# Kernel optimization log

Measured on AMD Instinct MI355X. Metric: run time of the kernel, lower is better.

The kernel has to match this reference:

```python
import jax, jax.numpy as jnp
import numpy as np

N = 4608      # total nodes (48 graphs x 96 nodes)
B = 48
NPG = 96
D = 512       # vec_dim
XD = 16       # x_dim
E = N * 32    # GAT edges
L = 6         # GAT layers


def _w(k, shape, fan_in):
    return jax.random.normal(k, shape, jnp.float32) * (1.0 / np.sqrt(fan_in))


def setup_inputs() -> dict:
    key = jax.random.key(0)
    ks = jax.random.split(key, 24)
    x = jax.random.normal(ks[0], (N, XD), jnp.float32)
    xyz = jax.random.normal(ks[1], (N, 3), jnp.float32)
    edge_index = jax.random.randint(ks[2], (2, E), 0, N, dtype=jnp.int32)
    ptr = (jnp.arange(B + 1) * NPG).astype(jnp.int32)
    # complete graph with replacement per segment (torch.combinations order: i<=j)
    i, j = np.triu_indices(NPG)
    offs = (np.arange(B) * NPG)[:, None]
    cloud_edge_index = jnp.asarray(
        np.stack([(i[None, :] + offs).reshape(-1), (j[None, :] + offs).reshape(-1)]),
        jnp.int32)
    return {
        'x': x, 'edge_index': edge_index, 'ptr': ptr, 'xyz': xyz,
        'cloud_edge_index': cloud_edge_index,
        'x_proj_w': _w(ks[3], (XD, D), XD), 'x_proj_b': jnp.zeros((D,), jnp.float32),
        'gat_wl': _w(ks[4], (L, D, D), D), 'gat_bl': jnp.zeros((L, D), jnp.float32),
        'gat_wr': _w(ks[5], (L, D, D), D), 'gat_br': jnp.zeros((L, D), jnp.float32),
        'gat_att': _w(ks[6], (L, D), D), 'gat_bias': jnp.zeros((L, D), jnp.float32),
        'gat_ln_g': jnp.ones((L - 1, D), jnp.float32), 'gat_ln_b': jnp.zeros((L - 1, D), jnp.float32),
        'cg_xyz_w': _w(ks[7], (3, D), 3),
        'cg_bn_g': jnp.ones((D,), jnp.float32), 'cg_bn_b': jnp.zeros((D,), jnp.float32),
        'cg_lin1_w': _w(ks[8], (D, D), D), 'cg_lin1_b': jnp.zeros((D,), jnp.float32),
        'cg_ln_g': jnp.ones((D,), jnp.float32), 'cg_ln_b': jnp.zeros((D,), jnp.float32),
        'lin_w': _w(ks[9], (D, D), D), 'lin_b': jnp.zeros((D,), jnp.float32),
        'bn_g': jnp.ones((D,), jnp.float32), 'bn_b': jnp.zeros((D,), jnp.float32),
    }


def _batchnorm(t, g, b):
    mu = t.mean(0)
    v = ((t - mu) ** 2).mean(0)
    return (t - mu) / jnp.sqrt(v + 1e-5) * g + b


def _forward(x, edge_index, cloud_edge_index, x_proj_w, x_proj_b, gat_wl, gat_bl,
             gat_wr, gat_br, gat_att, gat_bias, gat_ln_g, gat_ln_b, cg_xyz_w,
             cg_bn_g, cg_bn_b, cg_lin1_w, cg_lin1_b, cg_ln_g, cg_ln_b,
             lin_w, lin_b, bn_g, bn_b, xyz):
    n = x.shape[0]
    h = x @ x_proj_w + x_proj_b  # [N, D]
    # ---- GATv2 stack (heads=1, self-loops added, eval mode: no dropout) ----
    loops = jnp.arange(n, dtype=edge_index.dtype)
    ei = jnp.concatenate([edge_index, jnp.stack([loops, loops])], axis=1)
    src, dst = ei[0], ei[1]
    xg = h
    for l in range(L):
        xl = xg @ gat_wl[l] + gat_bl[l]
        xr = xg @ gat_wr[l] + gat_br[l]
        e = jax.nn.leaky_relu(xl[src] + xr[dst], 0.2) @ gat_att[l]  # [E+N]
        m = jax.ops.segment_max(e, dst, num_segments=n)
        ew = jnp.exp(e - m[dst])
        den = jax.ops.segment_sum(ew, dst, num_segments=n)
        alpha = ew / den[dst]
        out = jax.ops.segment_sum(alpha[:, None] * xl[src], dst, num_segments=n) + gat_bias[l]
        if l < L - 1:
            # PyG LayerNorm, mode='graph', batch=None: normalize over all elements
            mu = out.mean()
            sd = jnp.sqrt(((out - mu) ** 2).mean())
            out = (out - mu) / (sd + 1e-5) * gat_ln_g[l] + gat_ln_b[l]
            out = jax.nn.relu(out)
        xg = out
    # ---- CloudGraph (complete graph gather-compute-scatter) ----
    a, b = cloud_edge_index[0], cloud_edge_index[1]
    rx = h[a] - h[b]          # [Ec, D]
    rz = xyz[a] - xyz[b]      # [Ec, 3]
    sq = (rz ** 2).sum(-1)
    dist = jnp.where(sq > 0, jnp.sqrt(jnp.where(sq > 0, sq, 1.0)), 0.0)
    w = jnp.exp(-dist)[:, None]
    p1 = jax.ops.segment_sum(jax.nn.relu((w * rx) @ cg_lin1_w + cg_lin1_b), a, num_segments=n)
    mu1 = p1.mean(-1, keepdims=True)
    v1 = ((p1 - mu1) ** 2).mean(-1, keepdims=True)
    ln1 = (p1 - mu1) / jnp.sqrt(v1 + 1e-5) * cg_ln_g + cg_ln_b
    p2 = jax.ops.segment_sum(jax.nn.relu(rz @ cg_xyz_w), a, num_segments=n)
    xc = h + ln1 + _batchnorm(p2, cg_bn_g, cg_bn_b)
    # ---- fuse + final norm ----
    return _batchnorm((h + xg + xc) @ lin_w + lin_b, bn_g, bn_b)


def reference(x, edge_index, ptr, xyz, cloud_edge_index, x_proj_w, x_proj_b,
              gat_wl, gat_bl, gat_wr, gat_br, gat_att, gat_bias, gat_ln_g,
              gat_ln_b, cg_xyz_w, cg_bn_g, cg_bn_b, cg_lin1_w, cg_lin1_b,
              cg_ln_g, cg_ln_b, lin_w, lin_b, bn_g, bn_b):
    return _forward(x, edge_index, cloud_edge_index, x_proj_w, x_proj_b, gat_wl,
                    gat_bl, gat_wr, gat_br, gat_att, gat_bias, gat_ln_g,
                    gat_ln_b, cg_xyz_w, cg_bn_g, cg_bn_b, cg_lin1_w, cg_lin1_b,
                    cg_ln_g, cg_ln_b, lin_w, lin_b, bn_g, bn_b, xyz)
```

## Files before the change

kernel.cpp:

```cpp
#include <hip/hip_runtime.h>
#include <hip/hip_bf16.h>

#define NN 4608
#define BG 48
#define NPG 96
#define DD 512
#define XDIM 16
#define EREAL 147456
#define NLAYER 6
#define NK 262144
#define TRIU 4656

typedef __hip_bfloat16 bf16;
typedef short short8 __attribute__((ext_vector_type(8)));
typedef short shortx4 __attribute__((ext_vector_type(4)));
typedef float f32x4 __attribute__((ext_vector_type(4)));
typedef float f32x2 __attribute__((ext_vector_type(2)));

__device__ __forceinline__ float s2f(short s) {
  return __uint_as_float(((unsigned int)(unsigned short)s) << 16);
}
__device__ __forceinline__ short f2bs(float f) {
  bf16 h = __float2bfloat16(f);
  short s;
  __builtin_memcpy(&s, &h, 2);
  return s;
}
__device__ __forceinline__ void f8x4(unsigned int w, float* o) {
  f32x2 a = __builtin_amdgcn_cvt_pk_f32_fp8(w, false);
  f32x2 b = __builtin_amdgcn_cvt_pk_f32_fp8(w, true);
  o[0] = a[0]; o[1] = a[1]; o[2] = b[0]; o[3] = b[1];
}

typedef const __attribute__((address_space(1))) unsigned int ga_u32;
typedef __attribute__((address_space(3))) unsigned int ls_u32;
__device__ __forceinline__ void gl16(const void* g, void* l) {
  __builtin_amdgcn_global_load_lds((ga_u32*)g, (ls_u32*)l, 16, 0, 0);
}

__global__ __launch_bounds__(256) void k_wt(const float* __restrict__ wl,
                                            const float* __restrict__ wr,
                                            const float* __restrict__ cg,
                                            const float* __restrict__ lin,
                                            bf16* __restrict__ Wt,
                                            int* __restrict__ counts,
                                            float* __restrict__ statsAll) {
  if (blockIdx.z == 0) {
    int id = (blockIdx.y * 16 + blockIdx.x) * 256 + threadIdx.x;
    if (id < NN) counts[id] = 0;
    if (id < 5 * 32) statsAll[id] = 0.f;
  }
  __shared__ float tile[32][33];
  int z = blockIdx.z;
  const float* src = (z < 6) ? wl + (size_t)z * NK
                   : (z < 12) ? wr + (size_t)(z - 6) * NK
                   : (z == 12) ? cg : lin;
  bf16* dst = Wt + (size_t)z * NK;
  int c = threadIdx.x & 31;
  int r0 = threadIdx.x >> 5;
  int bx = blockIdx.x * 32, by = blockIdx.y * 32;
#pragma unroll
  for (int i = 0; i < 4; i++) {
    int r = r0 + i * 8;
    tile[r][c] = src[(size_t)(by + r) * 512 + bx + c];
  }
  __syncthreads();
#pragma unroll
  for (int i = 0; i < 4; i++) {
    int r = r0 + i * 8;
    dst[(size_t)(bx + r) * 512 + by + c] = __float2bfloat16(tile[c][r]);
  }
}

__global__ void k_xproj(const float* __restrict__ x, const float* __restrict__ w,
                        const float* __restrict__ b, const int* __restrict__ ei,
                        const float* __restrict__ xyz,
                        bf16* __restrict__ h_bf, int* __restrict__ counts,
                        float* __restrict__ ep) {
  int i = blockIdx.x * blockDim.x + threadIdx.x;
  if (i >= NN * DD) return;
  if (i < EREAL) atomicAdd(&counts[ei[EREAL + i]], 1);
  if (i < NN * NPG) {
    int n = i / NPG, e = i - n * NPG;
    int p = n % NPG;
    if (e < NPG - p) {
      int g = n / NPG;
      int slot = g * TRIU + p * NPG - (p * (p - 1)) / 2 + e;
      int j = n + e;
      float dx = xyz[n * 3] - xyz[j * 3];
      float dy = xyz[n * 3 + 1] - xyz[j * 3 + 1];
      float dz = xyz[n * 3 + 2] - xyz[j * 3 + 2];
      float sq = dx * dx + dy * dy + dz * dz;
      float dist = (sq > 0.f) ? sqrtf(sq) : 0.f;
      float4 v;
      v.x = dx; v.y = dy; v.z = dz; v.w = __expf(-dist);
      *(float4*)&ep[(size_t)slot * 4] = v;
    }
  }
  int n = i >> 9, d = i & 511;
  float acc = b[d];
#pragma unroll
  for (int k = 0; k < XDIM; k++) acc += x[n * XDIM + k] * w[k * DD + d];
  h_bf[i] = __float2bfloat16(acc);
}

__global__ void k_scan(const int* __restrict__ counts, int* offsets, int* cursor) {
  __shared__ int part[256];
  __shared__ int pre[256];
  int t = threadIdx.x;
  int base = t * 18;
  int s = 0;
#pragma unroll
  for (int i = 0; i < 18; i++) s += counts[base + i];
  part[t] = s;
  __syncthreads();
  if (t == 0) {
    int r = 0;
    for (int i = 0; i < 256; i++) { pre[i] = r; r += part[i]; }
  }
  __syncthreads();
  int run = pre[t];
#pragma unroll
  for (int i = 0; i < 18; i++) {
    offsets[base + i] = run;
    cursor[base + i] = run;
    run += counts[base + i];
  }
  if (t == 0) offsets[NN] = EREAL;
}
__global__ void k_scatter(const int* __restrict__ ei, int* cursor, int* ssrc) {
  int e = blockIdx.x * blockDim.x + threadIdx.x;
  if (e < EREAL) {
    int s = ei[e], d = ei[EREAL + e];
    int pos = atomicAdd(&cursor[d], 1);
    ssrc[pos] = s;
  }
}

__global__ __launch_bounds__(256) void k_ln(const bf16* __restrict__ in,
                                            bf16* __restrict__ out,
                                            const float* __restrict__ stats,
                                            const float* __restrict__ g,
                                            const float* __restrict__ b) {
  float s = 0.f, ss = 0.f;
#pragma unroll
  for (int i = 0; i < 16; i++) { s += stats[i]; ss += stats[16 + i]; }
  const float invM = 1.f / ((float)NN * (float)DD);
  float mu = s * invM;
  float var = ss * invM - mu * mu;
  float sd = sqrtf(fmaxf(var, 0.f));
  float inv = 1.f / (sd + 1e-5f);
  int i = blockIdx.x * 256 + threadIdx.x;
  int base = i * 8;
  int d0 = base & 511;
  short8 raw = *(const short8*)&in[base];
  short8 pk;
#pragma unroll
  for (int k = 0; k < 8; k++) {
    float t = fmaxf((s2f(raw[k]) - mu) * inv * g[d0 + k] + b[d0 + k], 0.f);
    pk[k] = f2bs(t);
  }
  *(short8*)&out[base] = pk;
}

__global__ __launch_bounds__(256) void k_gemm(
    const bf16* __restrict__ Abf,
    const bf16* __restrict__ B0, const bf16* __restrict__ B1,
    const float* __restrict__ bias0, const float* __restrict__ bias1,
    float* __restrict__ C0, float* __restrict__ C1,
    bf16* __restrict__ Cb0, bf16* __restrict__ Cb1,
    unsigned char* __restrict__ Cf8_0, unsigned char* __restrict__ Cf8_1,
    float* __restrict__ zptr, int zn,
    float* __restrict__ csum, float* __restrict__ csq, int nzl) {
  if (zptr && blockIdx.x == 0) {
    for (int i = threadIdx.x; i < zn; i += 256) zptr[i] = 0.f;
  }
  __shared__ __align__(16) bf16 As[2][128 * 64];
  __shared__ __align__(16) bf16 Bs[2][64 * 64];
  __shared__ float cs[64], cq[64];
  int cpx = gridDim.x >> 3;
  int wgid = (blockIdx.x & 7) * cpx + (blockIdx.x >> 3);
  int mi = wgid >> nzl;
  int r = wgid & ((1 << nzl) - 1);
  int z = r >> 3;
  int m0 = mi * 128, n0 = (r & 7) * 64;

  const bf16* B = z ? B1 : B0;
  const float* bias = z ? bias1 : bias0;
  float* C = z ? C1 : C0;
  bf16* Cb = z ? Cb1 : Cb0;
  unsigned char* Cf8 = z ? Cf8_1 : Cf8_0;
  int tid = threadIdx.x;
  int lane = tid & 63, wid = tid >> 6;
  int mh = (wid >> 1) * 64, nh = (wid & 1) * 32;
  int l15 = lane & 15, quad = lane >> 4;
  int lr8 = lane >> 3;
  int ls8 = lane & 7;
  int c16l = ls8 ^ (lr8 & 7);
  int swzr = (l15 & 7) * 8;

  if (csum && tid < 64) { cs[tid] = 0.f; cq[tid] = 0.f; }

  const bf16* aSrc = Abf + (size_t)(m0 + wid * 32 + lr8) * 512 + c16l * 8;
  const bf16* bSrc = B   + (size_t)(n0 + wid * 16 + lr8) * 512 + c16l * 8;

#define STAGE(bi, kt) do {                                              \
    gl16(aSrc + (kt) * 64,            &As[bi][(wid * 32     ) * 64]);   \
    gl16(aSrc + (kt) * 64 +  8 * 512, &As[bi][(wid * 32 +  8) * 64]);   \
    gl16(aSrc + (kt) * 64 + 16 * 512, &As[bi][(wid * 32 + 16) * 64]);   \
    gl16(aSrc + (kt) * 64 + 24 * 512, &As[bi][(wid * 32 + 24) * 64]);   \
    gl16(bSrc + (kt) * 64,            &Bs[bi][(wid * 16     ) * 64]);   \
    gl16(bSrc + (kt) * 64 +  8 * 512, &Bs[bi][(wid * 16 +  8) * 64]);   \
  } while (0)

  f32x4 acc[4][2];
#pragma unroll
  for (int mt = 0; mt < 4; mt++)
#pragma unroll
    for (int nt = 0; nt < 2; nt++) acc[mt][nt] = (f32x4)0.f;

  STAGE(0, 0);
  __syncthreads();

#pragma unroll
  for (int kt = 0; kt < 8; kt++) {
    const int cur = kt & 1;
    if (kt < 7) STAGE(cur ^ 1, kt + 1);
    short8 af[2][4], bfr[2][2];
#pragma unroll
    for (int kk = 0; kk < 2; kk++) {
#pragma unroll
      for (int mt = 0; mt < 4; mt++)
        af[kk][mt] = *(const short8*)&As[cur][(mh + mt * 16 + l15) * 64 +
                                             (((kk * 4 + quad) * 8) ^ swzr)];
#pragma unroll
      for (int nt = 0; nt < 2; nt++)
        bfr[kk][nt] = *(const short8*)&Bs[cur][(nh + nt * 16 + l15) * 64 +
                                              (((kk * 4 + quad) * 8) ^ swzr)];
    }
#pragma unroll
    for (int kk = 0; kk < 2; kk++)
#pragma unroll
      for (int mt = 0; mt < 4; mt++)
#pragma unroll
        for (int nt = 0; nt < 2; nt++)
          acc[mt][nt] = __builtin_amdgcn_mfma_f32_16x16x32_bf16(
              bfr[kk][nt], af[kk][mt], acc[mt][nt], 0, 0, 0);
    __syncthreads();
  }
#undef STAGE

  float colS[2][4] = {{0.f,0.f,0.f,0.f},{0.f,0.f,0.f,0.f}};
  float colQ[2][4] = {{0.f,0.f,0.f,0.f},{0.f,0.f,0.f,0.f}};
  float bv[2][4] = {{0.f,0.f,0.f,0.f},{0.f,0.f,0.f,0.f}};
#pragma unroll
  for (int nt = 0; nt < 2; nt++) {
    if (bias) {
      float4 b4 = *(const float4*)&bias[n0 + nh + nt * 16 + quad * 4];
      bv[nt][0] = b4.x; bv[nt][1] = b4.y; bv[nt][2] = b4.z; bv[nt][3] = b4.w;
    }
  }
#pragma unroll
  for (int mt = 0; mt < 4; mt++) {
    int row = m0 + mh + mt * 16 + l15;
#pragma unroll
    for (int nt = 0; nt < 2; nt++) {
      int col0 = n0 + nh + nt * 16 + quad * 4;
      float v[4];
#pragma unroll
      for (int r2 = 0; r2 < 4; r2++) {
        v[r2] = acc[mt][nt][r2] + bv[nt][r2];
        if (csum) { colS[nt][r2] += v[r2]; colQ[nt][r2] += v[r2] * v[r2]; }
      }
      if (C) {
        float4 o; o.x = v[0]; o.y = v[1]; o.z = v[2]; o.w = v[3];
        *(float4*)&C[(size_t)row * 512 + col0] = o;
      }
      if (Cb) {
        shortx4 o;
#pragma unroll
        for (int r2 = 0; r2 < 4; r2++) o[r2] = f2bs(v[r2]);
        *(shortx4*)&Cb[(size_t)row * 512 + col0] = o;
      }
      if (Cf8) {
        unsigned int u = __builtin_amdgcn_cvt_pk_fp8_f32(v[0], v[1], 0, false);
        u = __builtin_amdgcn_cvt_pk_fp8_f32(v[2], v[3], u, true);
        *(unsigned int*)&Cf8[(size_t)row * 512 + col0] = u;
      }
    }
  }
  if (csum) {
#pragma unroll
    for (int nt = 0; nt < 2; nt++)
#pragma unroll
      for (int r2 = 0; r2 < 4; r2++) {
        atomicAdd(&cs[nh + nt * 16 + quad * 4 + r2], colS[nt][r2]);
        atomicAdd(&cq[nh + nt * 16 + quad * 4 + r2], colQ[nt][r2]);
      }
    __syncthreads();
    if (tid < 64) {
      atomicAdd(&csum[n0 + tid], cs[tid]);
      atomicAdd(&csq[n0 + tid], cq[tid]);
    }
  }
}

__global__ __launch_bounds__(256) void k_gat_edge(const unsigned char* __restrict__ xl8,
                                                  const bf16* __restrict__ xr,
                                                  const float* __restrict__ att,
                                                  const float* __restrict__ bias,
                                                  const int* __restrict__ offs,
                                                  const int* __restrict__ ssrc,
                                                  bf16* __restrict__ out,
                                                  float* __restrict__ statsOut) {
  __shared__ float redS[4], redSS[4];
  int wave = (blockIdx.x * blockDim.x + threadIdx.x) >> 6;
  int lane = threadIdx.x & 63;
  int wid = threadIdx.x >> 6;
  if (wave < NN) {
    int n = wave;
    int base = lane * 8;
    float xrv[8], attv[8], acc[8];
    short8 xr8 = *(const short8*)&xr[(size_t)n * 512 + base];
#pragma unroll
    for (int k = 0; k < 8; k++) {
      xrv[k] = s2f(xr8[k]);
      attv[k] = att[base + k];
    }
    float m0, lsum;
    {
      uint2 q = *(const uint2*)&xl8[(size_t)n * 512 + base];
      float xs[8];
      f8x4(q.x, xs);
      f8x4(q.y, xs + 4);
      float sc0 = 0.f;
#pragma unroll
      for (int k = 0; k < 8; k++) {
        acc[k] = xs[k];
        float t = xs[k] + xrv[k];
        t = (t > 0.f) ? t : 0.2f * t;
        sc0 += attv[k] * t;
      }
#pragma unroll
      for (int off = 32; off >= 1; off >>= 1) sc0 += __shfl_xor(sc0, off, 64);
      m0 = sc0;
      lsum = 1.f;
    }
    int e0 = offs[n], e1 = offs[n + 1];
    int e = e0;
    for (; e + 3 < e1; e += 4) {
      int s0 = ssrc[e], s1 = ssrc[e + 1], s2 = ssrc[e + 2], s3 = ssrc[e + 3];
      uint2 q0 = *(const uint2*)&xl8[(size_t)s0 * 512 + base];
      uint2 q1 = *(const uint2*)&xl8[(size_t)s1 * 512 + base];
      uint2 q2 = *(const uint2*)&xl8[(size_t)s2 * 512 + base];
      uint2 q3 = *(const uint2*)&xl8[(size_t)s3 * 512 + base];
      float x0[8], x1[8], x2[8], x3[8];
      f8x4(q0.x, x0); f8x4(q0.y, x0 + 4);
      f8x4(q1.x, x1); f8x4(q1.y, x1 + 4);
      f8x4(q2.x, x2); f8x4(q2.y, x2 + 4);
      f8x4(q3.x, x3); f8x4(q3.y, x3 + 4);
      float c0 = 0.f, c1 = 0.f, c2 = 0.f, c3 = 0.f;
#pragma unroll
      for (int k = 0; k < 8; k++) {
        float t0 = x0[k] + xrv[k]; t0 = (t0 > 0.f) ? t0 : 0.2f * t0; c0 += attv[k] * t0;
        float t1 = x1[k] + xrv[k]; t1 = (t1 > 0.f) ? t1 : 0.2f * t1; c1 += attv[k] * t1;
        float t2 = x2[k] + xrv[k]; t2 = (t2 > 0.f) ? t2 : 0.2f * t2; c2 += attv[k] * t2;
        float t3 = x3[k] + xrv[k]; t3 = (t3 > 0.f) ? t3 : 0.2f * t3; c3 += attv[k] * t3;
      }
#pragma unroll
      for (int off = 32; off >= 1; off >>= 1) {
        c0 += __shfl_xor(c0, off, 64);
        c1 += __shfl_xor(c1, off, 64);
        c2 += __shfl_xor(c2, off, 64);
        c3 += __shfl_xor(c3, off, 64);
      }
      float p0 = __expf(c0 - m0), p1 = __expf(c1 - m0);
      float p2 = __expf(c2 - m0), p3 = __expf(c3 - m0);
      lsum += p0 + p1 + p2 + p3;
#pragma unroll
      for (int k = 0; k < 8; k++)
        acc[k] += p0 * x0[k] + p1 * x1[k] + p2 * x2[k] + p3 * x3[k];
    }
    for (; e < e1; ++e) {
      int s0 = ssrc[e];
      uint2 q = *(const uint2*)&xl8[(size_t)s0 * 512 + base];
      float x0[8];
      f8x4(q.x, x0);
      f8x4(q.y, x0 + 4);
      float sc0 = 0.f;
#pragma unroll
      for (int k = 0; k < 8; k++) {
        float t0 = x0[k] + xrv[k];
        t0 = (t0 > 0.f) ? t0 : 0.2f * t0;
        sc0 += attv[k] * t0;
      }
#pragma unroll
      for (int off = 32; off >= 1; off >>= 1) sc0 += __shfl_xor(sc0, off, 64);
      float p0 = __expf(sc0 - m0);
      lsum += p0;
#pragma unroll
      for (int k = 0; k < 8; k++) acc[k] += p0 * x0[k];
    }
    float inv = 1.f / lsum;
    float o[8];
    float s = 0.f, ss = 0.f;
    short8 o8;
#pragma unroll
    for (int k = 0; k < 8; k++) {
      o[k] = acc[k] * inv + bias[base + k];
      s += o[k];
      ss += o[k] * o[k];
      o8[k] = f2bs(o[k]);
    }
    *(short8*)&out[(size_t)n * 512 + base] = o8;
    if (statsOut) {
#pragma unroll
      for (int off = 32; off >= 1; off >>= 1) {
        s += __shfl_xor(s, off, 64);
        ss += __shfl_xor(ss, off, 64);
      }
      if (lane == 0) { redS[wid] = s; redSS[wid] = ss; }
    }
  }
  if (statsOut) {
    __syncthreads();
    if (threadIdx.x == 0) {
      float a = redS[0] + redS[1] + redS[2] + redS[3];
      float b = redSS[0] + redSS[1] + redSS[2] + redSS[3];
      int slot = blockIdx.x & 15;
      atomicAdd(&statsOut[slot], a);
      atomicAdd(&statsOut[16 + slot], b);
    }
  }
}

__global__ __launch_bounds__(256) void k_cloud(const bf16* __restrict__ g1,
                                               const float* __restrict__ ep,
                                               const float* __restrict__ lin1b,
                                               const float* __restrict__ w3,
                                               float* __restrict__ p1,
                                               float* __restrict__ p2) {
  int w = (blockIdx.x * blockDim.x + threadIdx.x) >> 6;
  int lane = threadIdx.x & 63;
  if (w >= NN * 2) return;
  int qf = w & 3;
  int pi = w >> 2;
  int g = pi / 48, pp = pi % 48;
  int d0 = qf * 128 + lane * 2;
  float bb0 = lin1b[d0], bb1 = lin1b[d0 + 1];
  float w00 = w3[d0], w01 = w3[d0 + 1];
  float w10 = w3[512 + d0], w11 = w3[512 + d0 + 1];
  float w20 = w3[1024 + d0], w21 = w3[1024 + d0 + 1];

#pragma unroll
  for (int half = 0; half < 2; half++) {
    int p = half ? (NPG - 1 - pp) : pp;
    int n = g * NPG + p;
    int cnt = NPG - p;
    int slot0 = g * TRIU + p * NPG - (p * (p - 1)) / 2;
    const bf16* grow = &g1[(size_t)n * 512 + d0];
    unsigned int giw = *(const unsigned int*)grow;
    float gi0 = s2f((short)(giw & 0xffff));
    float gi1 = s2f((short)(giw >> 16));
    float a10 = 0.f, a11 = 0.f, a20 = 0.f, a21 = 0.f;
    float b10 = 0.f, b11 = 0.f, b20 = 0.f, b21 = 0.f;
    int e = 0;
    for (; e + 3 < cnt; e += 4) {
      int sb = __builtin_amdgcn_readfirstlane(slot0 + e);
      float4 pa = *(const float4*)&ep[(size_t)sb * 4];
      float4 pb = *(const float4*)&ep[(size_t)(sb + 1) * 4];
      float4 pc = *(const float4*)&ep[(size_t)(sb + 2) * 4];
      float4 pd = *(const float4*)&ep[(size_t)(sb + 3) * 4];
      unsigned int ga = *(const unsigned int*)&grow[(size_t)e * 512];
      unsigned int gb = *(const unsigned int*)&grow[(size_t)(e + 1) * 512];
      unsigned int gc = *(const unsigned int*)&grow[(size_t)(e + 2) * 512];
      unsigned int gd = *(const unsigned int*)&grow[(size_t)(e + 3) * 512];
      float t;
      t = fmaf(pa.w, gi0 - s2f((short)(ga & 0xffff)), bb0); a10 += fmaxf(t, 0.f);
      t = fmaf(pa.w, gi1 - s2f((short)(ga >> 16)), bb1);    a11 += fmaxf(t, 0.f);
      t = fmaf(pb.w, gi0 - s2f((short)(gb & 0xffff)), bb0); b10 += fmaxf(t, 0.f);
      t = fmaf(pb.w, gi1 - s2f((short)(gb >> 16)), bb1);    b11 += fmaxf(t, 0.f);
      t = fmaf(pc.w, gi0 - s2f((short)(gc & 0xffff)), bb0); a10 += fmaxf(t, 0.f);
      t = fmaf(pc.w, gi1 - s2f((short)(gc >> 16)), bb1);    a11 += fmaxf(t, 0.f);
      t = fmaf(pd.w, gi0 - s2f((short)(gd & 0xffff)), bb0); b10 += fmaxf(t, 0.f);
      t = fmaf(pd.w, gi1 - s2f((short)(gd >> 16)), bb1);    b11 += fmaxf(t, 0.f);
      t = pa.x * w00 + pa.y * w10 + pa.z * w20; a20 += fmaxf(t, 0.f);
      t = pa.x * w01 + pa.y * w11 + pa.z * w21; a21 += fmaxf(t, 0.f);
      t = pb.x * w00 + pb.y * w10 + pb.z * w20; b20 += fmaxf(t, 0.f);
      t = pb.x * w01 + pb.y * w11 + pb.z * w21; b21 += fmaxf(t, 0.f);
      t = pc.x * w00 + pc.y * w10 + pc.z * w20; a20 += fmaxf(t, 0.f);
      t = pc.x * w01 + pc.y * w11 + pc.z * w21; a21 += fmaxf(t, 0.f);
      t = pd.x * w00 + pd.y * w10 + pd.z * w20; b20 += fmaxf(t, 0.f);
      t = pd.x * w01 + pd.y * w11 + pd.z * w21; b21 += fmaxf(t, 0.f);
    }
    for (; e < cnt; ++e) {
      float4 pa = *(const float4*)&ep[(size_t)(slot0 + e) * 4];
      unsigned int ga = *(const unsigned int*)&grow[(size_t)e * 512];
      float t;
      t = fmaf(pa.w, gi0 - s2f((short)(ga & 0xffff)), bb0); a10 += fmaxf(t, 0.f);
      t = fmaf(pa.w, gi1 - s2f((short)(ga >> 16)), bb1);    a11 += fmaxf(t, 0.f);
      t = pa.x * w00 + pa.y * w10 + pa.z * w20; a20 += fmaxf(t, 0.f);
      t = pa.x * w01 + pa.y * w11 + pa.z * w21; a21 += fmaxf(t, 0.f);
    }
    float2 o1, o2;
    o1.x = a10 + b10; o1.y = a11 + b11;
    o2.x = a20 + b20; o2.y = a21 + b21;
    *(float2*)&p1[(size_t)n * 512 + d0] = o1;
    *(float2*)&p2[(size_t)n * 512 + d0] = o2;
  }
}

__global__ __launch_bounds__(256) void k_cloud_epi(
    const float* __restrict__ p1, const float* __restrict__ p2,
    const bf16* __restrict__ h_bf, const bf16* __restrict__ xg_bf,
    const float* __restrict__ colsum, const float* __restrict__ colsq,
    const float* __restrict__ lng, const float* __restrict__ lnb,
    const float* __restrict__ bng, const float* __restrict__ bnb,
    bf16* __restrict__ s_bf, float* __restrict__ zptr) {
  if (blockIdx.x == 0) {
    for (int i = threadIdx.x; i < 1024; i += 256) zptr[i] = 0.f;
  }
  int wave = (blockIdx.x * blockDim.x + threadIdx.x) >> 6;
  int lane = threadIdx.x & 63;
  if (wave >= NN) return;
  int n = wave;
  size_t rb = (size_t)n * 512 + lane * 8;
  int base = lane * 8;
  float v[8];
  float s = 0.f;
#pragma unroll
  for (int k = 0; k < 8; k++) {
    v[k] = p1[rb + k];
    s += v[k];
  }
#pragma unroll
  for (int off = 32; off >= 1; off >>= 1) s += __shfl_xor(s, off, 64);
  float mu = s * (1.f / 512.f);
  float ss = 0.f;
#pragma unroll
  for (int k = 0; k < 8; k++) {
    float t = v[k] - mu;
    ss += t * t;
  }
#pragma unroll
  for (int off = 32; off >= 1; off >>= 1) ss += __shfl_xor(ss, off, 64);
  float inv = 1.f / sqrtf(ss * (1.f / 512.f) + 1e-5f);
  short8 hb = *(const short8*)&h_bf[rb];
  short8 xb = *(const short8*)&xg_bf[rb];
  short8 o8;
#pragma unroll
  for (int k = 0; k < 8; k++) {
    int d = base + k;
    float ln1 = (v[k] - mu) * inv * lng[d] + lnb[d];
    float cmu = colsum[d] * (1.f / NN);
    float cvar = colsq[d] * (1.f / NN) - cmu * cmu;
    float cinv = 1.f / sqrtf(fmaxf(cvar, 0.f) + 1e-5f);
    float bnv = (p2[rb + k] - cmu) * cinv * bng[d] + bnb[d];
    float out = 2.f * s2f(hb[k]) + s2f(xb[k]) + ln1 + bnv;
    o8[k] = f2bs(out);
  }
  *(short8*)&s_bf[rb] = o8;
}

__global__ void k_col_reduce(const float* __restrict__ x, float* colsum, float* colsq) {
  int r0 = blockIdx.x * 128;
  int c0 = threadIdx.x;
  float s0 = 0.f, q0 = 0.f, s1 = 0.f, q1 = 0.f;
  for (int r = r0; r < r0 + 128; ++r) {
    float v = x[(size_t)r * 512 + c0];
    s0 += v;
    q0 += v * v;
    float w = x[(size_t)r * 512 + c0 + 256];
    s1 += w;
    q1 += w * w;
  }
  atomicAdd(&colsum[c0], s0);
  atomicAdd(&colsq[c0], q0);
  atomicAdd(&colsum[c0 + 256], s1);
  atomicAdd(&colsq[c0 + 256], q1);
}
__global__ void k_bn_out(const float* __restrict__ y, const float* __restrict__ colsum,
                         const float* __restrict__ colsq, const float* __restrict__ g,
                         const float* __restrict__ b, float* __restrict__ out) {
  int i = blockIdx.x * blockDim.x + threadIdx.x;
  if (i >= NN * DD) return;
  int d = i & 511;
  float mu = colsum[d] * (1.f / NN);
  float var = colsq[d] * (1.f / NN) - mu * mu;
  float inv = 1.f / sqrtf(fmaxf(var, 0.f) + 1e-5f);
  out[i] = (y[i] - mu) * inv * g[d] + b[d];
}

extern "C" void kernel_launch(void* const* d_in, const int* in_sizes, int n_in,
                              void* d_out, int out_size, void* d_ws, size_t ws_size,
                              hipStream_t stream) {
  const float* x = (const float*)d_in[0];
  const int* ei = (const int*)d_in[1];
  const float* xyz = (const float*)d_in[3];
  const float* x_proj_w = (const float*)d_in[5];
  const float* x_proj_b = (const float*)d_in[6];
  const float* gat_wl = (const float*)d_in[7];
  const float* gat_bl = (const float*)d_in[8];
  const float* gat_wr = (const float*)d_in[9];
  const float* gat_br = (const float*)d_in[10];
  const float* gat_att = (const float*)d_in[11];
  const float* gat_bias = (const float*)d_in[12];
  const float* gat_ln_g = (const float*)d_in[13];
  const float* gat_ln_b = (const float*)d_in[14];
  const float* cg_xyz_w = (const float*)d_in[15];
  const float* cg_bn_g = (const float*)d_in[16];
  const float* cg_bn_b = (const float*)d_in[17];
  const float* cg_lin1_w = (const float*)d_in[18];
  const float* cg_lin1_b = (const float*)d_in[19];
  const float* cg_ln_g = (const float*)d_in[20];
  const float* cg_ln_b = (const float*)d_in[21];
  const float* lin_w = (const float*)d_in[22];
  const float* lin_b = (const float*)d_in[23];
  const float* bn_g = (const float*)d_in[24];
  const float* bn_b = (const float*)d_in[25];

  const size_t ND = (size_t)NN * DD;
  char* w = (char*)d_ws;
  float* p1 = (float*)w;       w += ND * 4;
  float* p2 = (float*)w;       w += ND * 4;
  bf16* h_bf = (bf16*)w;       w += ND * 2;
  bf16* xg_bf = (bf16*)w;      w += ND * 2;
  bf16* g1_bf = (bf16*)w;      w += ND * 2;
  bf16* xr_bf = (bf16*)w;      w += ND * 2;
  unsigned char* xl_f8 = (unsigned char*)w; w += ND;
  bf16* Wt = (bf16*)w;         w += (size_t)14 * NK * 2;
  float* eparam = (float*)w;   w += (size_t)BG * TRIU * 16;
  int* counts = (int*)w;       w += NN * 4;
  int* offs = (int*)w;         w += (NN + 4) * 4;
  int* cursor = (int*)w;       w += NN * 4;
  int* ssrc = (int*)w;         w += EREAL * 4;
  float* statsAll = (float*)w; w += 5 * 32 * 4;
  float* colsum = (float*)w;   w += 512 * 4;
  float* colsq = (float*)w;    w += 512 * 4;
  float* colsum2 = (float*)w;  w += 512 * 4;
  float* colsq2 = (float*)w;   w += 512 * 4;
  float* y = p1;
  bf16* s_bf = h_bf;
  bf16* aln_bf = g1_bf;

  const int TPB = 256;
  const int ND_BLK = (int)((ND + TPB - 1) / TPB);

  k_wt<<<dim3(16, 16, 14), TPB, 0, stream>>>(gat_wl, gat_wr, cg_lin1_w, lin_w, Wt,
                                             counts, statsAll);
  k_xproj<<<ND_BLK, TPB, 0, stream>>>(x, x_proj_w, x_proj_b, ei, xyz, h_bf,
                                      counts, eparam);
  k_scan<<<1, 256, 0, stream>>>(counts, offs, cursor);
  k_scatter<<<(EREAL + TPB - 1) / TPB, TPB, 0, stream>>>(ei, cursor, ssrc);

  for (int l = 0; l < NLAYER; l++) {
    const bf16* A;
    if (l == 0) {
      A = h_bf;
    } else {
      k_ln<<<(int)(ND / 8 / TPB), TPB, 0, stream>>>(
          xg_bf, aln_bf, statsAll + 32 * (l - 1),
          gat_ln_g + (size_t)(l - 1) * DD, gat_ln_b + (size_t)(l - 1) * DD);
      A = aln_bf;
    }
    k_gemm<<<576, TPB, 0, stream>>>(
        A, Wt + (size_t)l * NK, Wt + (size_t)(6 + l) * NK,
        gat_bl + l * DD, gat_br + l * DD, nullptr, nullptr, nullptr, xr_bf,
        xl_f8, nullptr, nullptr, 0, nullptr, nullptr, 4);
    float* sOut = (l < NLAYER - 1) ? statsAll + 32 * l : nullptr;
    k_gat_edge<<<NN / 4, TPB, 0, stream>>>(xl_f8, xr_bf, gat_att + l * DD,
                                           gat_bias + l * DD, offs, ssrc,
                                           xg_bf, sOut);
  }

  k_gemm<<<288, TPB, 0, stream>>>(
      h_bf, Wt + (size_t)12 * NK, Wt + (size_t)12 * NK, nullptr, nullptr,
      nullptr, nullptr, g1_bf, g1_bf, nullptr, nullptr,
      colsum, 1024, nullptr, nullptr, 3);
  k_cloud<<<NN / 2, TPB, 0, stream>>>(g1_bf, eparam, cg_lin1_b, cg_xyz_w, p1, p2);
  k_col_reduce<<<36, 256, 0, stream>>>(p2, colsum, colsq);
  k_cloud_epi<<<NN / 4, TPB, 0, stream>>>(p1, p2, h_bf, xg_bf, colsum, colsq,
                                          cg_ln_g, cg_ln_b, cg_bn_g, cg_bn_b,
                                          s_bf, colsum2);

  k_gemm<<<288, TPB, 0, stream>>>(
      s_bf, Wt + (size_t)13 * NK, Wt + (size_t)13 * NK, lin_b, lin_b,
      y, y, nullptr, nullptr, nullptr, nullptr,
      nullptr, 0, colsum2, colsq2, 3);
  k_bn_out<<<ND_BLK, TPB, 0, stream>>>(y, colsum2, colsq2, bn_g, bn_b,
                                       (float*)d_out);
}
```

Measured before the change: 545.3 us.

## Fuse six GAT layers into one persistent kernel with grid barriers

After: 1.699 ms. 3.11x slower.

```diff
diff --git a/kernel.cpp b/kernel.cpp
--- a/kernel.cpp
+++ b/kernel.cpp
@@ -10,6 +10,7 @@
 #define NLAYER 6
 #define NK 262144
 #define TRIU 4656
+#define MGRID 576
 
 typedef __hip_bfloat16 bf16;
 typedef short short8 __attribute__((ext_vector_type(8)));
@@ -36,6 +37,26 @@
 typedef __attribute__((address_space(3))) unsigned int ls_u32;
 __device__ __forceinline__ void gl16(const void* g, void* l) {
   __builtin_amdgcn_global_load_lds((ga_u32*)g, (ls_u32*)l, 16, 0, 0);
+}
+
+__device__ __forceinline__ void gsync(int* bar) {
+  __syncthreads();
+  if (threadIdx.x == 0) {
+    int* cnt = bar;
+    int* gen = bar + 16;
+    int g = __hip_atomic_load(gen, __ATOMIC_RELAXED, __HIP_MEMORY_SCOPE_AGENT);
+    __threadfence();
+    if (__hip_atomic_fetch_add(cnt, 1, __ATOMIC_ACQ_REL, __HIP_MEMORY_SCOPE_AGENT)
+        == (int)gridDim.x - 1) {
+      __hip_atomic_store(cnt, 0, __ATOMIC_RELAXED, __HIP_MEMORY_SCOPE_AGENT);
+      __hip_atomic_fetch_add(gen, 1, __ATOMIC_ACQ_REL, __HIP_MEMORY_SCOPE_AGENT);
+    } else {
+      while (__hip_atomic_load(gen, __ATOMIC_RELAXED, __HIP_MEMORY_SCOPE_AGENT) == g)
+        __builtin_amdgcn_s_sleep(1);
+      __hip_atomic_fetch_add(gen, 0, __ATOMIC_ACQUIRE, __HIP_MEMORY_SCOPE_AGENT);
+    }
+  }
+  __syncthreads();
 }
 
 __global__ __launch_bounds__(256) void k_wt(const float* __restrict__ wl,
@@ -104,7 +125,8 @@
   h_bf[i] = __float2bfloat16(acc);
 }
 
-__global__ void k_scan(const int* __restrict__ counts, int* offsets, int* cursor) {
+__global__ void k_scan(const int* __restrict__ counts, int* offsets, int* cursor,
+                       int* bar) {
   __shared__ int part[256];
   __shared__ int pre[256];
   int t = threadIdx.x;
@@ -126,7 +148,7 @@
     cursor[base + i] = run;
     run += counts[base + i];
   }
-  if (t == 0) offsets[NN] = EREAL;
+  if (t == 0) { offsets[NN] = EREAL; bar[0] = 0; }
 }
 __global__ void k_scatter(const int* __restrict__ ei, int* cursor, int* ssrc) {
   int e = blockIdx.x * blockDim.x + threadIdx.x;
@@ -137,30 +159,265 @@
   }
 }
 
-__global__ __launch_bounds__(256) void k_ln(const bf16* __restrict__ in,
-                                            bf16* __restrict__ out,
-                                            const float* __restrict__ stats,
-                                            const float* __restrict__ g,
-                                            const float* __restrict__ b) {
-  float s = 0.f, ss = 0.f;
-#pragma unroll
-  for (int i = 0; i < 16; i++) { s += stats[i]; ss += stats[16 + i]; }
-  const float invM = 1.f / ((float)NN * (float)DD);
-  float mu = s * invM;
-  float var = ss * invM - mu * mu;
-  float sd = sqrtf(fmaxf(var, 0.f));
-  float inv = 1.f / (sd + 1e-5f);
-  int i = blockIdx.x * 256 + threadIdx.x;
-  int base = i * 8;
-  int d0 = base & 511;
-  short8 raw = *(const short8*)&in[base];
-  short8 pk;
-#pragma unroll
-  for (int k = 0; k < 8; k++) {
-    float t = fmaxf((s2f(raw[k]) - mu) * inv * g[d0 + k] + b[d0 + k], 0.f);
-    pk[k] = f2bs(t);
-  }
-  *(short8*)&out[base] = pk;
+__global__ __launch_bounds__(256, 3) void k_mega(
+    const bf16* __restrict__ h_bf, bf16* __restrict__ xg_bf,
+    bf16* __restrict__ aln_bf, bf16* __restrict__ xr_bf,
+    unsigned char* __restrict__ xl_f8, const bf16* __restrict__ Wt,
+    const float* __restrict__ gat_bl, const float* __restrict__ gat_br,
+    const float* __restrict__ gat_att, const float* __restrict__ gat_bias,
+    const float* __restrict__ lng_all, const float* __restrict__ lnb_all,
+    const int* __restrict__ offs, const int* __restrict__ ssrc,
+    float* __restrict__ statsAll, int* __restrict__ bar) {
+  __shared__ __align__(16) bf16 As[2][128 * 64];
+  __shared__ __align__(16) bf16 Bs[2][64 * 64];
+  int tid = threadIdx.x;
+  int lane = tid & 63, wid = tid >> 6;
+  int cpx = gridDim.x >> 3;
+  int wgid = (blockIdx.x & 7) * cpx + (blockIdx.x >> 3);
+  int mi = wgid >> 4;
+  int rr = wgid & 15;
+  int z = rr >> 3;
+  int m0 = mi * 128, n0 = (rr & 7) * 64;
+  int mh = (wid >> 1) * 64, nh = (wid & 1) * 32;
+  int l15 = lane & 15, quad = lane >> 4;
+  int lr8 = lane >> 3, ls8 = lane & 7;
+  int c16l = ls8 ^ lr8;
+  int swzr = (l15 & 7) * 8;
+
+  for (int l = 0; l < NLAYER; l++) {
+    const bf16* A = h_bf;
+    if (l > 0) {
+      const float* st = statsAll + 32 * (l - 1);
+      float s = 0.f, ssum = 0.f;
+#pragma unroll
+      for (int i = 0; i < 16; i++) { s += st[i]; ssum += st[16 + i]; }
+      const float invM = 1.f / ((float)NN * (float)DD);
+      float mu = s * invM;
+      float var = ssum * invM - mu * mu;
+      float sd = sqrtf(fmaxf(var, 0.f));
+      float inv = 1.f / (sd + 1e-5f);
+      const float* g = lng_all + (size_t)(l - 1) * DD;
+      const float* b = lnb_all + (size_t)(l - 1) * DD;
+      int ci = blockIdx.x * 256 + tid;
+#pragma unroll
+      for (int rep = 0; rep < 2; rep++) {
+        int basei = (ci + rep * (MGRID * 256)) * 8;
+        int d0 = basei & 511;
+        short8 raw = *(const short8*)&xg_bf[basei];
+        short8 pk;
+#pragma unroll
+        for (int k = 0; k < 8; k++) {
+          float t = fmaxf((s2f(raw[k]) - mu) * inv * g[d0 + k] + b[d0 + k], 0.f);
+          pk[k] = f2bs(t);
+        }
+        *(short8*)&aln_bf[basei] = pk;
+      }
+      A = aln_bf;
+      gsync(bar);
+    }
+    {
+      const bf16* B = Wt + (size_t)(z ? 6 + l : l) * NK;
+      const float* bias = z ? (gat_br + (size_t)l * DD) : (gat_bl + (size_t)l * DD);
+      const bf16* aSrc = A + (size_t)(m0 + wid * 32 + lr8) * 512 + c16l * 8;
+      const bf16* bSrc = B + (size_t)(n0 + wid * 16 + lr8) * 512 + c16l * 8;
+
+#define STAGE(bi, kt) do {                                              \
+    gl16(aSrc + (kt) * 64,            &As[bi][(wid * 32     ) * 64]);   \
+    gl16(aSrc + (kt) * 64 +  8 * 512, &As[bi][(wid * 32 +  8) * 64]);   \
+    gl16(aSrc + (kt) * 64 + 16 * 512, &As[bi][(wid * 32 + 16) * 64]);   \
+    gl16(aSrc + (kt) * 64 + 24 * 512, &As[bi][(wid * 32 + 24) * 64]);   \
+    gl16(bSrc + (kt) * 64,            &Bs[bi][(wid * 16     ) * 64]);   \
+    gl16(bSrc + (kt) * 64 +  8 * 512, &Bs[bi][(wid * 16 +  8) * 64]);   \
+  } while (0)
+
+      f32x4 acc[4][2];
+#pragma unroll
+      for (int mt = 0; mt < 4; mt++)
+#pragma unroll
+        for (int nt = 0; nt < 2; nt++) acc[mt][nt] = (f32x4)0.f;
+
+      STAGE(0, 0);
+      __syncthreads();
+
+#pragma unroll
+      for (int kt = 0; kt < 8; kt++) {
+        const int cur = kt & 1;
+        if (kt < 7) STAGE(cur ^ 1, kt + 1);
+        short8 af[2][4], bfr[2][2];
+#pragma unroll
+        for (int kk = 0; kk < 2; kk++) {
+#pragma unroll
+          for (int mt = 0; mt < 4; mt++)
+            af[kk][mt] = *(const short8*)&As[cur][(mh + mt * 16 + l15) * 64 +
+                                                 (((kk * 4 + quad) * 8) ^ swzr)];
+#pragma unroll
+          for (int nt = 0; nt < 2; nt++)
+            bfr[kk][nt] = *(const short8*)&Bs[cur][(nh + nt * 16 + l15) * 64 +
+                                                  (((kk * 4 + quad) * 8) ^ swzr)];
+        }
+#pragma unroll
+        for (int kk = 0; kk < 2; kk++)
+#pragma unroll
+          for (int mt = 0; mt < 4; mt++)
+#pragma unroll
+            for (int nt = 0; nt < 2; nt++)
+              acc[mt][nt] = __builtin_amdgcn_mfma_f32_16x16x32_bf16(
+                  bfr[kk][nt], af[kk][mt], acc[mt][nt], 0, 0, 0);
+        __syncthreads();
+      }
+#undef STAGE
+
+      float bv[2][4];
+#pragma unroll
+      for (int nt = 0; nt < 2; nt++) {
+        float4 b4 = *(const float4*)&bias[n0 + nh + nt * 16 + quad * 4];
+        bv[nt][0] = b4.x; bv[nt][1] = b4.y; bv[nt][2] = b4.z; bv[nt][3] = b4.w;
+      }
+#pragma unroll
+      for (int mt = 0; mt < 4; mt++) {
+        int row = m0 + mh + mt * 16 + l15;
+#pragma unroll
+        for (int nt = 0; nt < 2; nt++) {
+          int col0 = n0 + nh + nt * 16 + quad * 4;
+          float v[4];
+#pragma unroll
+          for (int r2 = 0; r2 < 4; r2++) v[r2] = acc[mt][nt][r2] + bv[nt][r2];
+          if (z) {
+            shortx4 o;
+#pragma unroll
+            for (int r2 = 0; r2 < 4; r2++) o[r2] = f2bs(v[r2]);
+            *(shortx4*)&xr_bf[(size_t)row * 512 + col0] = o;
+          } else {
+            unsigned int u = __builtin_amdgcn_cvt_pk_fp8_f32(v[0], v[1], 0, false);
+            u = __builtin_amdgcn_cvt_pk_fp8_f32(v[2], v[3], u, true);
+            *(unsigned int*)&xl_f8[(size_t)row * 512 + col0] = u;
+          }
+        }
+      }
+    }
+    gsync(bar);
+    {
+      int wgl = blockIdx.x * 4 + wid;
+      int basei = lane * 8;
+      const float* att = gat_att + (size_t)l * DD;
+      const float* bias = gat_bias + (size_t)l * DD;
+      float attv[8], bv8[8];
+#pragma unroll
+      for (int k = 0; k < 8; k++) { attv[k] = att[basei + k]; bv8[k] = bias[basei + k]; }
+      float sAll = 0.f, ssAll = 0.f;
+#pragma unroll
+      for (int half = 0; half < 2; half++) {
+        int n = wgl + half * 2304;
+        float xrv[8], acc[8];
+        short8 xr8 = *(const short8*)&xr_bf[(size_t)n * 512 + basei];
+#pragma unroll
+        for (int k = 0; k < 8; k++) xrv[k] = s2f(xr8[k]);
+        float sm0, lsum;
+        {
+          uint2 q = *(const uint2*)&xl_f8[(size_t)n * 512 + basei];
+          float xs[8];
+          f8x4(q.x, xs);
+          f8x4(q.y, xs + 4);
+          float sc0 = 0.f;
+#pragma unroll
+          for (int k = 0; k < 8; k++) {
+            acc[k] = xs[k];
+            float t = xs[k] + xrv[k];
+            t = (t > 0.f) ? t : 0.2f * t;
+            sc0 += attv[k] * t;
+          }
+#pragma unroll
+          for (int off = 32; off >= 1; off >>= 1) sc0 += __shfl_xor(sc0, off, 64);
+          sm0 = sc0;
+          lsum = 1.f;
+        }
+        int e0 = offs[n], e1 = offs[n + 1];
+        int e = e0;
+        for (; e + 3 < e1; e += 4) {
+          int s0 = ssrc[e], s1 = ssrc[e + 1], s2 = ssrc[e + 2], s3 = ssrc[e + 3];
+          uint2 q0 = *(const uint2*)&xl_f8[(size_t)s0 * 512 + basei];
+          uint2 q1 = *(const uint2*)&xl_f8[(size_t)s1 * 512 + basei];
+          uint2 q2 = *(const uint2*)&xl_f8[(size_t)s2 * 512 + basei];
+          uint2 q3 = *(const uint2*)&xl_f8[(size_t)s3 * 512 + basei];
+          float x0[8], x1[8], x2[8], x3[8];
+          f8x4(q0.x, x0); f8x4(q0.y, x0 + 4);
+          f8x4(q1.x, x1); f8x4(q1.y, x1 + 4);
+          f8x4(q2.x, x2); f8x4(q2.y, x2 + 4);
+          f8x4(q3.x, x3); f8x4(q3.y, x3 + 4);
+          float c0 = 0.f, c1 = 0.f, c2 = 0.f, c3 = 0.f;
+#pragma unroll
+          for (int k = 0; k < 8; k++) {
+            float t0 = x0[k] + xrv[k]; t0 = (t0 > 0.f) ? t0 : 0.2f * t0; c0 += attv[k] * t0;
+            float t1 = x1[k] + xrv[k]; t1 = (t1 > 0.f) ? t1 : 0.2f * t1; c1 += attv[k] * t1;
+            float t2 = x2[k] + xrv[k]; t2 = (t2 > 0.f) ? t2 : 0.2f * t2; c2 += attv[k] * t2;
+            float t3 = x3[k] + xrv[k]; t3 = (t3 > 0.f) ? t3 : 0.2f * t3; c3 += attv[k] * t3;
+          }
+#pragma unroll
+          for (int off = 32; off >= 1; off >>= 1) {
+            c0 += __shfl_xor(c0, off, 64);
+            c1 += __shfl_xor(c1, off, 64);
+            c2 += __shfl_xor(c2, off, 64);
+            c3 += __shfl_xor(c3, off, 64);
+          }
+          float p0 = __expf(c0 - sm0), p1 = __expf(c1 - sm0);
+          float p2 = __expf(c2 - sm0), p3 = __expf(c3 - sm0);
+          lsum += p0 + p1 + p2 + p3;
+#pragma unroll
+          for (int k = 0; k < 8; k++)
+            acc[k] += p0 * x0[k] + p1 * x1[k] + p2 * x2[k] + p3 * x3[k];
+        }
+        for (; e < e1; ++e) {
+          int s0 = ssrc[e];
+          uint2 q = *(const uint2*)&xl_f8[(size_t)s0 * 512 + basei];
+          float x0[8];
+          f8x4(q.x, x0);
+          f8x4(q.y, x0 + 4);
+          float sc0 = 0.f;
+#pragma unroll
+          for (int k = 0; k < 8; k++) {
+            float t0 = x0[k] + xrv[k];
+            t0 = (t0 > 0.f) ? t0 : 0.2f * t0;
+            sc0 += attv[k] * t0;
+          }
+#pragma unroll
+          for (int off = 32; off >= 1; off >>= 1) sc0 += __shfl_xor(sc0, off, 64);
+          float p0 = __expf(sc0 - sm0);
+          lsum += p0;
+#pragma unroll
+          for (int k = 0; k < 8; k++) acc[k] += p0 * x0[k];
+        }
+        float inv = 1.f / lsum;
+        short8 o8;
+#pragma unroll
+        for (int k = 0; k < 8; k++) {
+          float o = acc[k] * inv + bv8[k];
+          sAll += o;
+          ssAll += o * o;
+          o8[k] = f2bs(o);
+        }
+        *(short8*)&xg_bf[(size_t)n * 512 + basei] = o8;
+      }
+      if (l < NLAYER - 1) {
+#pragma unroll
+        for (int off = 32; off >= 1; off >>= 1) {
+          sAll += __shfl_xor(sAll, off, 64);
+          ssAll += __shfl_xor(ssAll, off, 64);
+        }
+        float* red = (float*)&As[0][0];
+        __syncthreads();
+        if (lane == 0) { red[wid] = sAll; red[4 + wid] = ssAll; }
+        __syncthreads();
+        if (tid == 0) {
+          float a = red[0] + red[1] + red[2] + red[3];
+          float bq = red[4] + red[5] + red[6] + red[7];
+          int slot = blockIdx.x & 15;
+          atomicAdd(&statsAll[32 * l + slot], a);
+          atomicAdd(&statsAll[32 * l + 16 + slot], bq);
+        }
+        gsync(bar);
+      }
+    }
+  }
 }
 
 __global__ __launch_bounds__(256) void k_gemm(
@@ -301,135 +558,6 @@
     if (tid < 64) {
       atomicAdd(&csum[n0 + tid], cs[tid]);
       atomicAdd(&csq[n0 + tid], cq[tid]);
-    }
-  }
-}
-
-__global__ __launch_bounds__(256) void k_gat_edge(const unsigned char* __restrict__ xl8,
-                                                  const bf16* __restrict__ xr,
-                                                  const float* __restrict__ att,
-                                                  const float* __restrict__ bias,
-                                                  const int* __restrict__ offs,
-                                                  const int* __restrict__ ssrc,
-                                                  bf16* __restrict__ out,
-                                                  float* __restrict__ statsOut) {
-  __shared__ float redS[4], redSS[4];
-  int wave = (blockIdx.x * blockDim.x + threadIdx.x) >> 6;
-  int lane = threadIdx.x & 63;
-  int wid = threadIdx.x >> 6;
-  if (wave < NN) {
-    int n = wave;
-    int base = lane * 8;
-    float xrv[8], attv[8], acc[8];
-    short8 xr8 = *(const short8*)&xr[(size_t)n * 512 + base];
-#pragma unroll
-    for (int k = 0; k < 8; k++) {
-      xrv[k] = s2f(xr8[k]);
-      attv[k] = att[base + k];
-    }
-    float m0, lsum;
-    {
-      uint2 q = *(const uint2*)&xl8[(size_t)n * 512 + base];
-      float xs[8];
-      f8x4(q.x, xs);
-      f8x4(q.y, xs + 4);
-      float sc0 = 0.f;
-#pragma unroll
-      for (int k = 0; k < 8; k++) {
-        acc[k] = xs[k];
-        float t = xs[k] + xrv[k];
-        t = (t > 0.f) ? t : 0.2f * t;
-        sc0 += attv[k] * t;
-      }
-#pragma unroll
-      for (int off = 32; off >= 1; off >>= 1) sc0 += __shfl_xor(sc0, off, 64);
-      m0 = sc0;
-      lsum = 1.f;
-    }
-    int e0 = offs[n], e1 = offs[n + 1];
-    int e = e0;
-    for (; e + 3 < e1; e += 4) {
-      int s0 = ssrc[e], s1 = ssrc[e + 1], s2 = ssrc[e + 2], s3 = ssrc[e + 3];
-      uint2 q0 = *(const uint2*)&xl8[(size_t)s0 * 512 + base];
-      uint2 q1 = *(const uint2*)&xl8[(size_t)s1 * 512 + base];
-      uint2 q2 = *(const uint2*)&xl8[(size_t)s2 * 512 + base];
-      uint2 q3 = *(const uint2*)&xl8[(size_t)s3 * 512 + base];
-      float x0[8], x1[8], x2[8], x3[8];
-      f8x4(q0.x, x0); f8x4(q0.y, x0 + 4);
-      f8x4(q1.x, x1); f8x4(q1.y, x1 + 4);
-      f8x4(q2.x, x2); f8x4(q2.y, x2 + 4);
-      f8x4(q3.x, x3); f8x4(q3.y, x3 + 4);
-      float c0 = 0.f, c1 = 0.f, c2 = 0.f, c3 = 0.f;
-#pragma unroll
-      for (int k = 0; k < 8; k++) {
-        float t0 = x0[k] + xrv[k]; t0 = (t0 > 0.f) ? t0 : 0.2f * t0; c0 += attv[k] * t0;
-        float t1 = x1[k] + xrv[k]; t1 = (t1 > 0.f) ? t1 : 0.2f * t1; c1 += attv[k] * t1;
-        float t2 = x2[k] + xrv[k]; t2 = (t2 > 0.f) ? t2 : 0.2f * t2; c2 += attv[k] * t2;
-        float t3 = x3[k] + xrv[k]; t3 = (t3 > 0.f) ? t3 : 0.2f * t3; c3 += attv[k] * t3;
-      }
-#pragma unroll
-      for (int off = 32; off >= 1; off >>= 1) {
-        c0 += __shfl_xor(c0, off, 64);
-        c1 += __shfl_xor(c1, off, 64);
-        c2 += __shfl_xor(c2, off, 64);
-        c3 += __shfl_xor(c3, off, 64);
-      }
-      float p0 = __expf(c0 - m0), p1 = __expf(c1 - m0);
-      float p2 = __expf(c2 - m0), p3 = __expf(c3 - m0);
-      lsum += p0 + p1 + p2 + p3;
-#pragma unroll
-      for (int k = 0; k < 8; k++)
-        acc[k] += p0 * x0[k] + p1 * x1[k] + p2 * x2[k] + p3 * x3[k];
-    }
-    for (; e < e1; ++e) {
-      int s0 = ssrc[e];
-      uint2 q = *(const uint2*)&xl8[(size_t)s0 * 512 + base];
-      float x0[8];
-      f8x4(q.x, x0);
-      f8x4(q.y, x0 + 4);
-      float sc0 = 0.f;
-#pragma unroll
-      for (int k = 0; k < 8; k++) {
-        float t0 = x0[k] + xrv[k];
-        t0 = (t0 > 0.f) ? t0 : 0.2f * t0;
-        sc0 += attv[k] * t0;
-      }
-#pragma unroll
-      for (int off = 32; off >= 1; off >>= 1) sc0 += __shfl_xor(sc0, off, 64);
-      float p0 = __expf(sc0 - m0);
-      lsum += p0;
-#pragma unroll
-      for (int k = 0; k < 8; k++) acc[k] += p0 * x0[k];
-    }
-    float inv = 1.f / lsum;
-    float o[8];
-    float s = 0.f, ss = 0.f;
-    short8 o8;
-#pragma unroll
-    for (int k = 0; k < 8; k++) {
-      o[k] = acc[k] * inv + bias[base + k];
-      s += o[k];
-      ss += o[k] * o[k];
-      o8[k] = f2bs(o[k]);
-    }
-    *(short8*)&out[(size_t)n * 512 + base] = o8;
-    if (statsOut) {
-#pragma unroll
-      for (int off = 32; off >= 1; off >>= 1) {
-        s += __shfl_xor(s, off, 64);
-        ss += __shfl_xor(ss, off, 64);
-      }
-      if (lane == 0) { redS[wid] = s; redSS[wid] = ss; }
-    }
-  }
-  if (statsOut) {
-    __syncthreads();
-    if (threadIdx.x == 0) {
-      float a = redS[0] + redS[1] + redS[2] + redS[3];
-      float b = redSS[0] + redSS[1] + redSS[2] + redSS[3];
-      int slot = blockIdx.x & 15;
-      atomicAdd(&statsOut[slot], a);
-      atomicAdd(&statsOut[16 + slot], b);
     }
   }
 }
@@ -639,6 +767,7 @@
   float* colsq = (float*)w;    w += 512 * 4;
   float* colsum2 = (float*)w;  w += 512 * 4;
   float* colsq2 = (float*)w;   w += 512 * 4;
+  int* bar = (int*)w;          w += 64 * 4;
   float* y = p1;
   bf16* s_bf = h_bf;
   bf16* aln_bf = g1_bf;
@@ -650,28 +779,13 @@
                                              counts, statsAll);
   k_xproj<<<ND_BLK, TPB, 0, stream>>>(x, x_proj_w, x_proj_b, ei, xyz, h_bf,
                                       counts, eparam);
-  k_scan<<<1, 256, 0, stream>>>(counts, offs, cursor);
+  k_scan<<<1, 256, 0, stream>>>(counts, offs, cursor, bar);
   k_scatter<<<(EREAL + TPB - 1) / TPB, TPB, 0, stream>>>(ei, cursor, ssrc);
 
-  for (int l = 0; l < NLAYER; l++) {
-    const bf16* A;
-    if (l == 0) {
-      A = h_bf;
-    } else {
-      k_ln<<<(int)(ND / 8 / TPB), TPB, 0, stream>>>(
-          xg_bf, aln_bf, statsAll + 32 * (l - 1),
-          gat_ln_g + (size_t)(l - 1) * DD, gat_ln_b + (size_t)(l - 1) * DD);
-      A = aln_bf;
-    }
-    k_gemm<<<576, TPB, 0, stream>>>(
-        A, Wt + (size_t)l * NK, Wt + (size_t)(6 + l) * NK,
-        gat_bl + l * DD, gat_br + l * DD, nullptr, nullptr, nullptr, xr_bf,
-        xl_f8, nullptr, nullptr, 0, nullptr, nullptr, 4);
-    float* sOut = (l < NLAYER - 1) ? statsAll + 32 * l : nullptr;
-    k_gat_edge<<<NN / 4, TPB, 0, stream>>>(xl_f8, xr_bf, gat_att + l * DD,
-                                           gat_bias + l * DD, offs, ssrc,
-                                           xg_bf, sOut);
-  }
+  k_mega<<<MGRID, TPB, 0, stream>>>(h_bf, xg_bf, aln_bf, xr_bf, xl_f8, Wt,
+                                    gat_bl, gat_br, gat_att, gat_bias,
+                                    gat_ln_g, gat_ln_b, offs, ssrc,
+                                    statsAll, bar);
 
   k_gemm<<<288, TPB, 0, stream>>>(
       h_bf, Wt + (size_t)12 * NK, Wt + (size_t)12 * NK, nullptr, nullptr,
```
